# Kernel optimization log

Measured on AMD Instinct MI355X. Metric: run time of the kernel, lower is better.

Reference implementation:

```python
import jax, jax.numpy as jnp
import numpy as np

N = 50000      # nodes
E = 800000     # edges (before self-loops)
FEAT = 128     # input feature dim F
HID = 32       # per-head hidden H
HEADS = 8      # n_head
C = 40         # classes
NEG_SLOPE = 0.2


def setup_inputs() -> dict:
    key = jax.random.key(0)
    ks = jax.random.split(key, 12)
    x = jax.random.normal(ks[0], (N, FEAT), jnp.float32)
    edge_index = jax.random.randint(ks[1], (2, E), 0, N, jnp.int32)
    s1 = 1.0 / np.sqrt(FEAT)
    s2 = 1.0 / np.sqrt(HEADS * HID)
    W1 = jax.random.normal(ks[2], (FEAT, HEADS * HID), jnp.float32) * s1
    a1_src = jax.random.normal(ks[3], (HEADS, HID), jnp.float32) * s2
    a1_dst = jax.random.normal(ks[4], (HEADS, HID), jnp.float32) * s2
    b1 = jnp.zeros((HEADS * HID,), jnp.float32)
    W2 = jax.random.normal(ks[5], (HEADS * HID, HEADS * HID), jnp.float32) * s2
    a2_src = jax.random.normal(ks[6], (HEADS, HID), jnp.float32) * s2
    a2_dst = jax.random.normal(ks[7], (HEADS, HID), jnp.float32) * s2
    b2 = jnp.zeros((HEADS * HID,), jnp.float32)
    Wc = jax.random.normal(ks[8], (HEADS * HID, C), jnp.float32) * s2
    bc = jnp.zeros((C,), jnp.float32)
    return {"x": x, "edge_index": edge_index,
            "W1": W1, "a1_src": a1_src, "a1_dst": a1_dst, "b1": b1,
            "W2": W2, "a2_src": a2_src, "a2_dst": a2_dst, "b2": b2,
            "Wc": Wc, "bc": bc}


def gat_conv(x, src, dst, W, a_src, a_dst, b):
    # x: [N, F_in] -> per-head features [N, heads, H]
    n = x.shape[0]
    xh = (x @ W).reshape(n, HEADS, HID)
    alpha_s = jnp.einsum('nhd,hd->nh', xh, a_src)   # [N, heads]
    alpha_d = jnp.einsum('nhd,hd->nh', xh, a_dst)   # [N, heads]
    e = alpha_s[src] + alpha_d[dst]                  # [E, heads]
    e = jnp.where(e > 0, e, NEG_SLOPE * e)           # LeakyReLU(0.2)
    # softmax over incoming edges grouped by destination node
    emax = jax.ops.segment_max(e, dst, num_segments=n)
    ex = jnp.exp(e - emax[dst])
    denom = jax.ops.segment_sum(ex, dst, num_segments=n)
    alpha = ex / denom[dst]                          # [E, heads]
    msg = xh[src] * alpha[:, :, None]                # [E, heads, H]
    out = jax.ops.segment_sum(msg, dst, num_segments=n)
    return out.reshape(n, HEADS * HID) + b


def reference(x, edge_index, W1, a1_src, a1_dst, b1, W2, a2_src, a2_dst, b2, Wc, bc):
    # PyG GATConv adds self-loops by default
    loops = jnp.arange(N, dtype=edge_index.dtype)
    ei = jnp.concatenate([edge_index, jnp.stack([loops, loops])], axis=1)
    src, dst = ei[0], ei[1]
    h = gat_conv(x, src, dst, W1, a1_src, a1_dst, b1)
    h = jax.nn.relu(h)
    h = gat_conv(h, src, dst, W2, a2_src, a2_dst, b2)
    h = jax.nn.relu(h)
    return h @ Wc + bc
```

## Files before the change

### kernel.cpp

```cpp
#include <hip/hip_runtime.h>
#include <math.h>

#define NNODES 50000
#define NEDGES 800000
#define NTOT   850000
#define NHEAD  8
#define HDIM   32
#define HHD    256
#define NCLS   40
#define NEG_SLOPE 0.2f

typedef _Float16 half4 __attribute__((ext_vector_type(4)));
typedef _Float16 half8 __attribute__((ext_vector_type(8)));
typedef float f32x16 __attribute__((ext_vector_type(16)));
typedef unsigned short u16;


__global__ void k_init_counts(int* __restrict__ counts) {
    int i = blockIdx.x * 256 + threadIdx.x;
    if (i < NNODES) counts[i] = 1;
}

__global__ void k_count(const int* __restrict__ ei, int* __restrict__ counts) {
    int i = blockIdx.x * 256 + threadIdx.x;
    if (i < NEDGES) atomicAdd(&counts[ei[NEDGES + i]], 1);
}

__global__ __launch_bounds__(256) void k_scan1(const int* __restrict__ counts,
                                               int* __restrict__ partial,
                                               int* __restrict__ bsums) {
    __shared__ int lds[256];
    int t = threadIdx.x;
    int i = blockIdx.x * 256 + t;
    int v = (i < NNODES) ? counts[i] : 0;
    lds[t] = v;
    __syncthreads();
    for (int off = 1; off < 256; off <<= 1) {
        int add = (t >= off) ? lds[t - off] : 0;
        __syncthreads();
        lds[t] += add;
        __syncthreads();
    }
    if (i < NNODES) partial[i] = lds[t] - v;
    if (t == 255) bsums[blockIdx.x] = lds[255];
}

__global__ __launch_bounds__(256) void k_scan2(const int* __restrict__ bsums,
                                               int* __restrict__ boff, int nb) {
    __shared__ int lds[256];
    int t = threadIdx.x;
    int v = (t < nb) ? bsums[t] : 0;
    lds[t] = v;
    __syncthreads();
    for (int off = 1; off < 256; off <<= 1) {
        int add = (t >= off) ? lds[t - off] : 0;
        __syncthreads();
        lds[t] += add;
        __syncthreads();
    }
    if (t < nb) boff[t] = lds[t] - v;
}

__global__ void k_scan3(int* __restrict__ row_ptr, const int* __restrict__ boff,
                        int* __restrict__ cursor) {
    int i = blockIdx.x * 256 + threadIdx.x;
    if (i < NNODES) {
        int r = row_ptr[i] + boff[blockIdx.x];
        row_ptr[i] = r;
        cursor[i] = r;
    }
    if (i == 0) row_ptr[NNODES] = NTOT;
}

__global__ void k_scatter(const int* __restrict__ ei, int* __restrict__ cursor,
                          int* __restrict__ esrc) {
    int i = blockIdx.x * 256 + threadIdx.x;
    if (i < NEDGES) {
        int s = ei[i];
        int d = ei[NEDGES + i];
        int pos = atomicAdd(&cursor[d], 1);
        esrc[pos] = s;
    } else if (i < NTOT) {
        int n = i - NEDGES;
        int pos = atomicAdd(&cursor[n], 1);
        esrc[pos] = n;
    }
}

__global__ void k_prep_all(const float* __restrict__ W1, const float* __restrict__ W2,
                           const float* __restrict__ Wc,
                           _Float16* __restrict__ w1t, _Float16* __restrict__ w2t,
                           _Float16* __restrict__ wct) {
    int gid = blockIdx.x * 256 + threadIdx.x;
    if (gid >= 256 * 64) return;
    int frag = gid >> 6, l = gid & 63;
    const float* W; _Float16* Wt; int K, Nc, fkn, fbase;
    if (frag < 64)       { W = W1; Wt = w1t; K = 128; Nc = 256; fkn = 8;  fbase = 0; }
    else if (frag < 192) { W = W2; Wt = w2t; K = 256; Nc = 256; fkn = 16; fbase = 64; }
    else                 { W = Wc; Wt = wct; K = 256; Nc = 40;  fkn = 16; fbase = 192; }
    int f = frag - fbase;
    int fn = f / fkn, fk = f - fn * fkn;
    int n = fn * 32 + (l & 31);
    int k = fk * 16 + ((l >> 5) << 3);
    half8 v;
    #pragma unroll
    for (int j = 0; j < 8; ++j)
        v[j] = (n < Nc) ? (_Float16)W[(size_t)(k + j) * Nc + n] : (_Float16)0.f;
    *reinterpret_cast<half8*>(Wt + ((size_t)f * 64 + l) * 8) = v;
}

#define TBM 128
#define TBN 128
#define TBK 32
#define APAD 34

template <typename AT, int K, int MODE>
__global__ __launch_bounds__(256) void k_mfma_gemm(
    const AT* __restrict__ A,
    const _Float16* __restrict__ Wt,
    _Float16* __restrict__ Ch,
    float* __restrict__ Cf,
    const float* __restrict__ bias,
    const float* __restrict__ a_src,
    const float* __restrict__ a_dst,
    float* __restrict__ alpha_s,
    float* __restrict__ alpha_d,
    int M, int ldc)
{
    constexpr bool A_IS_F32 = sizeof(AT) == 4;
    __shared__ _Float16 Ah[TBM][APAD];
    __shared__ _Float16 Ct[(MODE == 0) ? TBM : 1][TBN + 4];
    int t = threadIdx.x;
    int lane = t & 63;
    int wid = t >> 6;
    int wr = wid >> 1, wc = wid & 1;
    int rowBase = blockIdx.y * TBM;
    int colBase = blockIdx.x * TBN;

    int arow = t >> 1;
    int akoff = (t & 1) * 16;
    bool arow_ok = (rowBase + arow) < M;
    const AT* aptr = A + (size_t)(rowBase + arow) * K + akoff;

    constexpr int FKN = K >> 4;
    size_t bbase[2];
    #pragma unroll
    for (int ct = 0; ct < 2; ++ct) {
        int fn = blockIdx.x * 4 + wc * 2 + ct;
        bbase[ct] = ((size_t)fn * FKN) * 512 + (size_t)lane * 8;
    }

    f32x16 acc[2][2];
    #pragma unroll
    for (int i = 0; i < 2; ++i)
        #pragma unroll
        for (int j = 0; j < 2; ++j)
            #pragma unroll
            for (int r = 0; r < 16; ++r) acc[i][j][r] = 0.f;

    float4 aregf[4];
    half8  aregh[2];
    auto load_a = [&](const AT* ap) {
        if constexpr (A_IS_F32) {
            #pragma unroll
            for (int i = 0; i < 4; ++i)
                aregf[i] = arow_ok ? *reinterpret_cast<const float4*>((const float*)ap + i * 4)
                                   : float4{0.f, 0.f, 0.f, 0.f};
        } else {
            #pragma unroll
            for (int i = 0; i < 2; ++i)
                aregh[i] = arow_ok ? *reinterpret_cast<const half8*>((const _Float16*)ap + i * 8)
                                   : half8{0, 0, 0, 0, 0, 0, 0, 0};
        }
    };
    load_a(aptr);

    half8 bf0[2], bf1[2];
    #pragma unroll
    for (int ct = 0; ct < 2; ++ct) {
        bf0[ct] = *reinterpret_cast<const half8*>(Wt + bbase[ct]);
        bf1[ct] = *reinterpret_cast<const half8*>(Wt + bbase[ct] + 512);
    }

    #pragma unroll
    for (int k0 = 0; k0 < K; k0 += TBK) {
        if constexpr (A_IS_F32) {
            half8 h0, h1;
            #pragma unroll
            for (int c = 0; c < 4; ++c) {
                float4 v = aregf[c];
                if (c < 2) {
                    h0[c * 4 + 0] = (_Float16)v.x; h0[c * 4 + 1] = (_Float16)v.y;
                    h0[c * 4 + 2] = (_Float16)v.z; h0[c * 4 + 3] = (_Float16)v.w;
                } else {
                    h1[(c - 2) * 4 + 0] = (_Float16)v.x; h1[(c - 2) * 4 + 1] = (_Float16)v.y;
                    h1[(c - 2) * 4 + 2] = (_Float16)v.z; h1[(c - 2) * 4 + 3] = (_Float16)v.w;
                }
            }
            *reinterpret_cast<half8*>(&Ah[arow][akoff])     = h0;
            *reinterpret_cast<half8*>(&Ah[arow][akoff + 8]) = h1;
        } else {
            *reinterpret_cast<half8*>(&Ah[arow][akoff])     = aregh[0];
            *reinterpret_cast<half8*>(&Ah[arow][akoff + 8]) = aregh[1];
        }
        __syncthreads();
        if (k0 + TBK < K) load_a(aptr + k0 + TBK);
        half8 bn0[2], bn1[2];
        if (k0 + TBK < K) {
            #pragma unroll
            for (int ct = 0; ct < 2; ++ct) {
                size_t nb = bbase[ct] + (size_t)((k0 >> 4) + 2) * 512;
                bn0[ct] = *reinterpret_cast<const half8*>(Wt + nb);
                bn1[ct] = *reinterpret_cast<const half8*>(Wt + nb + 512);
            }
        }
        #pragma unroll
        for (int sub = 0; sub < 2; ++sub) {
            int kfo = sub * 16 + (lane >> 5) * 8;
            half8 ah[2];
            #pragma unroll
            for (int rt = 0; rt < 2; ++rt) {
                int r = wr * 64 + rt * 32 + (lane & 31);
                ah[rt] = *reinterpret_cast<const half8*>(&Ah[r][kfo]);
            }
            #pragma unroll
            for (int rt = 0; rt < 2; ++rt)
                #pragma unroll
                for (int ct = 0; ct < 2; ++ct)
                    acc[rt][ct] = __builtin_amdgcn_mfma_f32_32x32x16_f16(
                        ah[rt], (sub == 0) ? bf0[ct] : bf1[ct], acc[rt][ct], 0, 0, 0);
        }
        if (k0 + TBK < K) {
            #pragma unroll
            for (int ct = 0; ct < 2; ++ct) { bf0[ct] = bn0[ct]; bf1[ct] = bn1[ct]; }
        }
        __syncthreads();
    }

    #pragma unroll
    for (int rt = 0; rt < 2; ++rt)
        #pragma unroll
        for (int ct = 0; ct < 2; ++ct) {
            int lcol = wc * 64 + ct * 32 + (lane & 31);
            int col = colBase + lcol;
            #pragma unroll
            for (int r = 0; r < 16; ++r) {
                int lrow = wr * 64 + rt * 32 + (r & 3) + 8 * (r >> 2) + 4 * (lane >> 5);
                int row = rowBase + lrow;
                float v = acc[rt][ct][r];
                if constexpr (MODE == 0) {
                    _Float16 hv = (_Float16)v;
                    Ct[lrow][lcol] = hv;
                    if (row < M)
                        Ch[(size_t)row * ldc + col] = hv;
                } else {
                    if (row < M && col < NCLS)
                        Cf[(size_t)row * ldc + col] = v + bias[col];
                }
            }
        }

    if constexpr (MODE == 0) {
        __syncthreads();
        #pragma unroll
        for (int idx = t; idx < TBM * 4; idx += 256) {
            int lrow = idx >> 2, hoff = idx & 3;
            int grow = rowBase + lrow;
            if (grow < M) {
                int h = blockIdx.x * 4 + hoff;
                const float* as4 = a_src + h * HDIM;
                const float* ad4 = a_dst + h * HDIM;
                float ss = 0.f, sd = 0.f;
                #pragma unroll
                for (int j = 0; j < HDIM; ++j) {
                    float v = (float)Ct[lrow][hoff * 32 + j];
                    ss += v * as4[j];
                    sd += v * ad4[j];
                }
                alpha_s[grow * NHEAD + h] = ss;
                alpha_d[grow * NHEAD + h] = sd;
            }
        }
    }
}

__global__ __launch_bounds__(256) void k_agg(const _Float16* __restrict__ xh,
                                             const float* __restrict__ alpha_s,
                                             const float* __restrict__ alpha_d,
                                             const int* __restrict__ row_ptr,
                                             const int* __restrict__ esrc,
                                             const float* __restrict__ bias,
                                             _Float16* __restrict__ out) {
    int wave = blockIdx.x * 4 + (threadIdx.x >> 6);
    int node = wave * 2 + ((threadIdx.x & 63) >> 5);
    if (node >= NNODES) return;
    int l = threadIdx.x & 31;
    int h = l >> 2;
    int beg = row_ptr[node], end = row_ptr[node + 1];
    float ad = alpha_d[node * NHEAD + h];
    float acc[8] = {};
    float ssum = 0.f;
    int i = beg;
    for (; i + 3 < end; i += 4) {
        int s0 = esrc[i], s1 = esrc[i + 1], s2 = esrc[i + 2], s3 = esrc[i + 3];
        float e0 = alpha_s[s0 * NHEAD + h] + ad;
        float e1 = alpha_s[s1 * NHEAD + h] + ad;
        float e2 = alpha_s[s2 * NHEAD + h] + ad;
        float e3 = alpha_s[s3 * NHEAD + h] + ad;
        half8 v0 = *reinterpret_cast<const half8*>(xh + (size_t)s0 * HHD + l * 8);
        half8 v1 = *reinterpret_cast<const half8*>(xh + (size_t)s1 * HHD + l * 8);
        half8 v2 = *reinterpret_cast<const half8*>(xh + (size_t)s2 * HHD + l * 8);
        half8 v3 = *reinterpret_cast<const half8*>(xh + (size_t)s3 * HHD + l * 8);
        e0 = (e0 > 0.f) ? e0 : NEG_SLOPE * e0;
        e1 = (e1 > 0.f) ? e1 : NEG_SLOPE * e1;
        e2 = (e2 > 0.f) ? e2 : NEG_SLOPE * e2;
        e3 = (e3 > 0.f) ? e3 : NEG_SLOPE * e3;
        float p0 = __expf(e0), p1 = __expf(e1), p2 = __expf(e2), p3 = __expf(e3);
        ssum += (p0 + p1) + (p2 + p3);
        #pragma unroll
        for (int d = 0; d < 8; ++d)
            acc[d] += p0 * (float)v0[d] + p1 * (float)v1[d] +
                      p2 * (float)v2[d] + p3 * (float)v3[d];
    }
    for (; i < end; ++i) {
        int s0 = esrc[i];
        float e0 = alpha_s[s0 * NHEAD + h] + ad;
        half8 v0 = *reinterpret_cast<const half8*>(xh + (size_t)s0 * HHD + l * 8);
        e0 = (e0 > 0.f) ? e0 : NEG_SLOPE * e0;
        float p0 = __expf(e0);
        ssum += p0;
        #pragma unroll
        for (int d = 0; d < 8; ++d)
            acc[d] += p0 * (float)v0[d];
    }
    float inv = 1.f / ssum;
    float4 b0 = *reinterpret_cast<const float4*>(bias + l * 8);
    float4 b1 = *reinterpret_cast<const float4*>(bias + l * 8 + 4);
    float bb[8] = {b0.x, b0.y, b0.z, b0.w, b1.x, b1.y, b1.z, b1.w};
    half8 r;
    #pragma unroll
    for (int d = 0; d < 8; ++d)
        r[d] = (_Float16)fmaxf(acc[d] * inv + bb[d], 0.f);
    *reinterpret_cast<half8*>(out + (size_t)node * HHD + l * 8) = r;
}


extern "C" void kernel_launch(void* const* d_in, const int* in_sizes, int n_in,
                              void* d_out, int out_size, void* d_ws, size_t ws_size,
                              hipStream_t stream) {
    const float* x   = (const float*)d_in[0];
    const int*   ei  = (const int*)  d_in[1];
    const float* W1  = (const float*)d_in[2];
    const float* a1s = (const float*)d_in[3];
    const float* a1d = (const float*)d_in[4];
    const float* b1  = (const float*)d_in[5];
    const float* W2  = (const float*)d_in[6];
    const float* a2s = (const float*)d_in[7];
    const float* a2d = (const float*)d_in[8];
    const float* b2  = (const float*)d_in[9];
    const float* Wc  = (const float*)d_in[10];
    const float* bc  = (const float*)d_in[11];
    float* out = (float*)d_out;

    char* ws = (char*)d_ws;
    size_t off = 0;
    auto alloc = [&](size_t bytes) -> void* {
        void* p = ws + off;
        off += (bytes + 255) & ~(size_t)255;
        return p;
    };
    _Float16* xh_h   = (_Float16*)alloc((size_t)NNODES * HHD * 2);
    _Float16* hbuf_h = (_Float16*)alloc((size_t)NNODES * HHD * 2);
    float* as_   = (float*)alloc((size_t)NNODES * NHEAD * 4);
    float* ad_   = (float*)alloc((size_t)NNODES * NHEAD * 4);
    int* counts  = (int*)alloc((size_t)NNODES * 4);
    int* row_ptr = (int*)alloc((size_t)(NNODES + 1) * 4);
    int* cursor  = (int*)alloc((size_t)NNODES * 4);
    int* esrc    = (int*)alloc((size_t)NTOT * 4);
    int* bsums   = (int*)alloc(256 * 4);
    int* boff    = (int*)alloc(256 * 4);
    _Float16* w1t = (_Float16*)alloc((size_t)64 * 64 * 8 * 2);
    _Float16* w2t = (_Float16*)alloc((size_t)128 * 64 * 8 * 2);
    _Float16* wct = (_Float16*)alloc((size_t)64 * 64 * 8 * 2);
    (void)ws_size; (void)in_sizes; (void)n_in; (void)out_size;

    int gn = (NNODES + 255) / 256;
    int ge = (NEDGES + 255) / 256;
    int gt = (NTOT + 255) / 256;

    k_init_counts<<<gn, 256, 0, stream>>>(counts);
    k_count<<<ge, 256, 0, stream>>>(ei, counts);
    k_scan1<<<gn, 256, 0, stream>>>(counts, row_ptr, bsums);
    k_scan2<<<1, 256, 0, stream>>>(bsums, boff, gn);
    k_scan3<<<gn, 256, 0, stream>>>(row_ptr, boff, cursor);
    k_scatter<<<gt, 256, 0, stream>>>(ei, cursor, esrc);

    k_prep_all<<<64, 256, 0, stream>>>(W1, W2, Wc, w1t, w2t, wct);

    dim3 gHid(HHD / TBN, (NNODES + TBM - 1) / TBM);
    dim3 gCls(1, (NNODES + TBM - 1) / TBM);
    int gagg = NNODES / 8;

    k_mfma_gemm<float, 128, 0><<<gHid, 256, 0, stream>>>(
        x, w1t, xh_h, nullptr, nullptr, a1s, a1d, as_, ad_, NNODES, HHD);
    k_agg<<<gagg, 256, 0, stream>>>(xh_h, as_, ad_, row_ptr, esrc, b1, hbuf_h);

    k_mfma_gemm<_Float16, 256, 0><<<gHid, 256, 0, stream>>>(
        hbuf_h, w2t, xh_h, nullptr, nullptr, a2s, a2d, as_, ad_, NNODES, HHD);
    k_agg<<<gagg, 256, 0, stream>>>(xh_h, as_, ad_, row_ptr, esrc, b2, hbuf_h);

    k_mfma_gemm<_Float16, 256, 1><<<gCls, 256, 0, stream>>>(
        hbuf_h, wct, nullptr, out, bc, nullptr, nullptr, nullptr, nullptr,
        NNODES, NCLS);
}
```

Before: 329.1 us.

## Halve GEMM row tile, share LDS buffer, and vectorize epilogue stores

Cuts the GEMM M-tile from 128 to 64 rows, so each wave computes a 32x64 tile with two accumulators instead of four. This doubles the number of blocks for better occupancy and CU fill on a 50k-row problem. The A-tile and output staging buffers now share a single LDS array, reducing LDS per block. The MODE 0 epilogue writes C through LDS as 16-byte row-contiguous half8 stores instead of scattered 2-byte stores. The trade-off is less MFMA reuse of each B fragment per block and more B-fragment reloads overall.

```diff
diff --git a/kernel.cpp b/kernel.cpp
--- a/kernel.cpp
+++ b/kernel.cpp
@@ -109,10 +109,11 @@
     *reinterpret_cast<half8*>(Wt + ((size_t)f * 64 + l) * 8) = v;
 }
 
-#define TBM 128
+#define TBM 64
 #define TBN 128
 #define TBK 32
 #define APAD 34
+#define LDCT 132
 
 template <typename AT, int K, int MODE>
 __global__ __launch_bounds__(256) void k_mfma_gemm(
@@ -128,8 +129,8 @@
     int M, int ldc)
 {
     constexpr bool A_IS_F32 = sizeof(AT) == 4;
-    __shared__ _Float16 Ah[TBM][APAD];
-    __shared__ _Float16 Ct[(MODE == 0) ? TBM : 1][TBN + 4];
+    constexpr int SMEM_ELEMS = (MODE == 0) ? TBM * LDCT : TBM * APAD;
+    __shared__ _Float16 smem[SMEM_ELEMS];
     int t = threadIdx.x;
     int lane = t & 63;
     int wid = t >> 6;
@@ -137,8 +138,8 @@
     int rowBase = blockIdx.y * TBM;
     int colBase = blockIdx.x * TBN;
 
-    int arow = t >> 1;
-    int akoff = (t & 1) * 16;
+    int arow = t >> 2;
+    int akoff = (t & 3) * 8;
     bool arow_ok = (rowBase + arow) < M;
     const AT* aptr = A + (size_t)(rowBase + arow) * K + akoff;
 
@@ -150,27 +151,23 @@
         bbase[ct] = ((size_t)fn * FKN) * 512 + (size_t)lane * 8;
     }
 
-    f32x16 acc[2][2];
-    #pragma unroll
-    for (int i = 0; i < 2; ++i)
-        #pragma unroll
-        for (int j = 0; j < 2; ++j)
-            #pragma unroll
-            for (int r = 0; r < 16; ++r) acc[i][j][r] = 0.f;
-
-    float4 aregf[4];
-    half8  aregh[2];
+    f32x16 acc[2];
+    #pragma unroll
+    for (int j = 0; j < 2; ++j)
+        #pragma unroll
+        for (int r = 0; r < 16; ++r) acc[j][r] = 0.f;
+
+    float4 aregf[2];
+    half8  aregh;
     auto load_a = [&](const AT* ap) {
         if constexpr (A_IS_F32) {
             #pragma unroll
-            for (int i = 0; i < 4; ++i)
+            for (int i = 0; i < 2; ++i)
                 aregf[i] = arow_ok ? *reinterpret_cast<const float4*>((const float*)ap + i * 4)
                                    : float4{0.f, 0.f, 0.f, 0.f};
         } else {
-            #pragma unroll
-            for (int i = 0; i < 2; ++i)
-                aregh[i] = arow_ok ? *reinterpret_cast<const half8*>((const _Float16*)ap + i * 8)
-                                   : half8{0, 0, 0, 0, 0, 0, 0, 0};
+            aregh = arow_ok ? *reinterpret_cast<const half8*>((const _Float16*)ap)
+                            : half8{0, 0, 0, 0, 0, 0, 0, 0};
         }
     };
     load_a(aptr);
@@ -184,25 +181,16 @@
 
     #pragma unroll
     for (int k0 = 0; k0 < K; k0 += TBK) {
+        half8 hv;
         if constexpr (A_IS_F32) {
-            half8 h0, h1;
-            #pragma unroll
-            for (int c = 0; c < 4; ++c) {
-                float4 v = aregf[c];
-                if (c < 2) {
-                    h0[c * 4 + 0] = (_Float16)v.x; h0[c * 4 + 1] = (_Float16)v.y;
-                    h0[c * 4 + 2] = (_Float16)v.z; h0[c * 4 + 3] = (_Float16)v.w;
-                } else {
-                    h1[(c - 2) * 4 + 0] = (_Float16)v.x; h1[(c - 2) * 4 + 1] = (_Float16)v.y;
-                    h1[(c - 2) * 4 + 2] = (_Float16)v.z; h1[(c - 2) * 4 + 3] = (_Float16)v.w;
-                }
-            }
-            *reinterpret_cast<half8*>(&Ah[arow][akoff])     = h0;
-            *reinterpret_cast<half8*>(&Ah[arow][akoff + 8]) = h1;
+            hv[0] = (_Float16)aregf[0].x; hv[1] = (_Float16)aregf[0].y;
+            hv[2] = (_Float16)aregf[0].z; hv[3] = (_Float16)aregf[0].w;
+            hv[4] = (_Float16)aregf[1].x; hv[5] = (_Float16)aregf[1].y;
+            hv[6] = (_Float16)aregf[1].z; hv[7] = (_Float16)aregf[1].w;
         } else {
-            *reinterpret_cast<half8*>(&Ah[arow][akoff])     = aregh[0];
-            *reinterpret_cast<half8*>(&Ah[arow][akoff + 8]) = aregh[1];
-        }
+            hv = aregh;
+        }
+        *reinterpret_cast<half8*>(&smem[arow * APAD + akoff]) = hv;
         __syncthreads();
         if (k0 + TBK < K) load_a(aptr + k0 + TBK);
         half8 bn0[2], bn1[2];
@@ -217,18 +205,12 @@
         #pragma unroll
         for (int sub = 0; sub < 2; ++sub) {
             int kfo = sub * 16 + (lane >> 5) * 8;
-            half8 ah[2];
-            #pragma unroll
-            for (int rt = 0; rt < 2; ++rt) {
-                int r = wr * 64 + rt * 32 + (lane & 31);
-                ah[rt] = *reinterpret_cast<const half8*>(&Ah[r][kfo]);
-            }
-            #pragma unroll
-            for (int rt = 0; rt < 2; ++rt)
-                #pragma unroll
-                for (int ct = 0; ct < 2; ++ct)
-                    acc[rt][ct] = __builtin_amdgcn_mfma_f32_32x32x16_f16(
-                        ah[rt], (sub == 0) ? bf0[ct] : bf1[ct], acc[rt][ct], 0, 0, 0);
+            half8 ah = *reinterpret_cast<const half8*>(
+                &smem[(wr * 32 + (lane & 31)) * APAD + kfo]);
+            #pragma unroll
+            for (int ct = 0; ct < 2; ++ct)
+                acc[ct] = __builtin_amdgcn_mfma_f32_32x32x16_f16(
+                    ah, (sub == 0) ? bf0[ct] : bf1[ct], acc[ct], 0, 0, 0);
         }
         if (k0 + TBK < K) {
             #pragma unroll
@@ -237,34 +219,30 @@
         __syncthreads();
     }
 
-    #pragma unroll
-    for (int rt = 0; rt < 2; ++rt)
+    if constexpr (MODE == 0) {
         #pragma unroll
         for (int ct = 0; ct < 2; ++ct) {
             int lcol = wc * 64 + ct * 32 + (lane & 31);
-            int col = colBase + lcol;
             #pragma unroll
             for (int r = 0; r < 16; ++r) {
-                int lrow = wr * 64 + rt * 32 + (r & 3) + 8 * (r >> 2) + 4 * (lane >> 5);
-                int row = rowBase + lrow;
-                float v = acc[rt][ct][r];
-                if constexpr (MODE == 0) {
-                    _Float16 hv = (_Float16)v;
-                    Ct[lrow][lcol] = hv;
-                    if (row < M)
-                        Ch[(size_t)row * ldc + col] = hv;
-                } else {
-                    if (row < M && col < NCLS)
-                        Cf[(size_t)row * ldc + col] = v + bias[col];
-                }
+                int lrow = wr * 32 + (r & 3) + 8 * (r >> 2) + 4 * (lane >> 5);
+                smem[lrow * LDCT + lcol] = (_Float16)acc[ct][r];
             }
         }
-
-    if constexpr (MODE == 0) {
-        __syncthreads();
-        #pragma unroll
-        for (int idx = t; idx < TBM * 4; idx += 256) {
-            int lrow = idx >> 2, hoff = idx & 3;
+        __syncthreads();
+        #pragma unroll
+        for (int pass = 0; pass < 4; ++pass) {
+            int idx = t + pass * 256;
+            int lrow = idx >> 4;
+            int cchunk = (idx & 15) * 8;
+            int grow = rowBase + lrow;
+            if (grow < M) {
+                half8 v = *reinterpret_cast<const half8*>(&smem[lrow * LDCT + cchunk]);
+                *reinterpret_cast<half8*>(Ch + (size_t)grow * ldc + colBase + cchunk) = v;
+            }
+        }
+        {
+            int lrow = t >> 2, hoff = t & 3;
             int grow = rowBase + lrow;
             if (grow < M) {
                 int h = blockIdx.x * 4 + hoff;
@@ -273,12 +251,23 @@
                 float ss = 0.f, sd = 0.f;
                 #pragma unroll
                 for (int j = 0; j < HDIM; ++j) {
-                    float v = (float)Ct[lrow][hoff * 32 + j];
+                    float v = (float)smem[lrow * LDCT + hoff * 32 + j];
                     ss += v * as4[j];
                     sd += v * ad4[j];
                 }
                 alpha_s[grow * NHEAD + h] = ss;
                 alpha_d[grow * NHEAD + h] = sd;
+            }
+        }
+    } else {
+        #pragma unroll
+        for (int ct = 0; ct < 2; ++ct) {
+            int col = colBase + wc * 64 + ct * 32 + (lane & 31);
+            #pragma unroll
+            for (int r = 0; r < 16; ++r) {
+                int row = rowBase + wr * 32 + (r & 3) + 8 * (r >> 2) + 4 * (lane >> 5);
+                if (row < M && col < NCLS)
+                    Cf[(size_t)row * ldc + col] = acc[ct][r] + bias[col];
             }
         }
     }
```

New measurement: 311.7 us. 1.06x faster.
